# Kernel tuning notes

Hardware: AMD Instinct MI355X
Metric: run time of the kernel (lower is better)

## Reference

```python
import jax, jax.numpy as jnp
import numpy as np

B, N, DIM, H, DH = 4, 2048, 768, 12, 64

def layer_norm_no_affine(x, eps=1e-5):
    mu = jnp.mean(x, axis=-1, keepdims=True)
    var = jnp.var(x, axis=-1, keepdims=True)
    return (x - mu) / jnp.sqrt(var + eps)

def setup_inputs() -> dict:
    key = jax.random.key(0)
    ks = jax.random.split(key, 6)
    s = 1.0 / np.sqrt(DIM)
    return {
        "x": jax.random.normal(ks[0], (B, N, DIM), dtype=jnp.float32),
        "gamma": jnp.zeros((DIM,), dtype=jnp.float32),
        "Wq": jax.random.normal(ks[1], (DIM, DIM), dtype=jnp.float32) * s,
        "Wk": jax.random.normal(ks[2], (DIM, DIM), dtype=jnp.float32) * s,
        "Wv": jax.random.normal(ks[3], (DIM, DIM), dtype=jnp.float32) * s,
        "Wo": jax.random.normal(ks[4], (DIM, DIM), dtype=jnp.float32) * s,
    }

def reference(x, gamma, Wq, Wk, Wv, Wo):
    scale = DH ** -0.5
    xn = layer_norm_no_affine(x) * (gamma + 1.0)  # [b,n,dim]
    # projections (torch Linear: y = x @ W.T), split heads b n (h d) -> b h n d
    def proj(t, W):
        return (t @ W.T).reshape(B, N, H, DH).transpose(0, 2, 1, 3)
    q = proj(xn, Wq) * scale
    k = proj(xn, Wk)
    v = proj(xn, Wv)
    qk_sim = jnp.einsum('bhid,bhjd->bhij', q, k)  # full N x N scores (unfused)
    attn = jax.nn.softmax(qk_sim, axis=-1)
    out = jnp.einsum('bhij,bhjd->bhid', attn, v)
    out = out.transpose(0, 2, 1, 3).reshape(B, N, H * DH)
    return out @ Wo.T
```

## Files before the change

### kernel.cpp

```cpp
#include <hip/hip_runtime.h>
#include <stdint.h>

#define NSEQ 2048
#define NB 4
#define NH 12
#define MTOT 8192
#define DMODEL 768

typedef __attribute__((ext_vector_type(8))) short bfx8;
typedef __attribute__((ext_vector_type(4))) float fx4;

static __device__ __forceinline__ unsigned short f2bf(float f) {
  union { float f; unsigned u; } v; v.f = f;
  unsigned r = v.u + 0x7FFFu + ((v.u >> 16) & 1u);
  return (unsigned short)(r >> 16);
}

static __device__ __forceinline__ unsigned cvt_pk_bf16(float lo, float hi) {
  unsigned r;
  asm("v_cvt_pk_bf16_f32 %0, %1, %2" : "=v"(r) : "v"(lo), "v"(hi));
  return r;
}

static __device__ __forceinline__ void gload_lds16(const void* g, void* l) {
  __builtin_amdgcn_global_load_lds(
      (const __attribute__((address_space(1))) unsigned int*)g,
      (__attribute__((address_space(3))) unsigned int*)l, 16, 0, 0);
}

__global__ __launch_bounds__(256) void k_ln(const float* __restrict__ x,
                                            const float* __restrict__ gamma,
                                            unsigned short* __restrict__ xn) {
  int row = blockIdx.x * 4 + (threadIdx.x >> 6);
  int lane = threadIdx.x & 63;
  const float* xr = x + (size_t)row * DMODEL;
  float4 a = *(const float4*)(xr + lane * 4);
  float4 b = *(const float4*)(xr + 256 + lane * 4);
  float4 c = *(const float4*)(xr + 512 + lane * 4);
  float s  = a.x + a.y + a.z + a.w + b.x + b.y + b.z + b.w + c.x + c.y + c.z + c.w;
  float ss = a.x*a.x + a.y*a.y + a.z*a.z + a.w*a.w
           + b.x*b.x + b.y*b.y + b.z*b.z + b.w*b.w
           + c.x*c.x + c.y*c.y + c.z*c.z + c.w*c.w;
  #pragma unroll
  for (int off = 1; off < 64; off <<= 1) {
    s  += __shfl_xor(s, off);
    ss += __shfl_xor(ss, off);
  }
  float mu = s * (1.0f / 768.0f);
  float var = ss * (1.0f / 768.0f) - mu * mu;
  float rs = rsqrtf(var + 1e-5f);
  float4 ga = *(const float4*)(gamma + lane * 4);
  float4 gb = *(const float4*)(gamma + 256 + lane * 4);
  float4 gc = *(const float4*)(gamma + 512 + lane * 4);
  unsigned short* orow = xn + (size_t)row * DMODEL;
  ushort4 o;
  o.x = f2bf((a.x - mu) * rs * (ga.x + 1.0f));
  o.y = f2bf((a.y - mu) * rs * (ga.y + 1.0f));
  o.z = f2bf((a.z - mu) * rs * (ga.z + 1.0f));
  o.w = f2bf((a.w - mu) * rs * (ga.w + 1.0f));
  *(ushort4*)(orow + lane * 4) = o;
  o.x = f2bf((b.x - mu) * rs * (gb.x + 1.0f));
  o.y = f2bf((b.y - mu) * rs * (gb.y + 1.0f));
  o.z = f2bf((b.z - mu) * rs * (gb.z + 1.0f));
  o.w = f2bf((b.w - mu) * rs * (gb.w + 1.0f));
  *(ushort4*)(orow + 256 + lane * 4) = o;
  o.x = f2bf((c.x - mu) * rs * (gc.x + 1.0f));
  o.y = f2bf((c.y - mu) * rs * (gc.y + 1.0f));
  o.z = f2bf((c.z - mu) * rs * (gc.z + 1.0f));
  o.w = f2bf((c.w - mu) * rs * (gc.w + 1.0f));
  *(ushort4*)(orow + 512 + lane * 4) = o;
}

__global__ __launch_bounds__(256) void k_wconv(const float* __restrict__ w0,
                                               const float* __restrict__ w1,
                                               const float* __restrict__ w2,
                                               const float* __restrict__ w3,
                                               unsigned short* __restrict__ dst) {
  int which = blockIdx.y;
  const float* src = (which == 0) ? w0 : (which == 1) ? w1 : (which == 2) ? w2 : w3;
  size_t idx = ((size_t)blockIdx.x * 256 + threadIdx.x) * 4;
  float4 v = *(const float4*)(src + idx);
  ushort4 o;
  o.x = f2bf(v.x); o.y = f2bf(v.y); o.z = f2bf(v.z); o.w = f2bf(v.w);
  *(ushort4*)(dst + (size_t)which * (DMODEL * DMODEL) + idx) = o;
}

template<int MODE>
__global__ __launch_bounds__(256) void k_gemm(const unsigned short* __restrict__ A,
                                              const unsigned short* __restrict__ Bbase,
                                              unsigned short* __restrict__ q_o,
                                              unsigned short* __restrict__ k_o,
                                              unsigned short* __restrict__ v_o,
                                              float* __restrict__ f_o) {
  __shared__ unsigned short At[128 * 32];
  __shared__ unsigned short Bt[128 * 32];
  int t = threadIdx.x;
  int w = t >> 6, lane = t & 63;
  int wr = w >> 1, wc = w & 1;
  int g = lane >> 4, cc = lane & 15;
  int mbase = blockIdx.x * 128;
  int by = blockIdx.y;
  const unsigned short* Bp;
  int ncolbase;
  if (MODE == 0) {
    int which = by / 6;
    Bp = Bbase + (size_t)which * (DMODEL * DMODEL);
    ncolbase = (by % 6) * 128;
  } else {
    Bp = Bbase;
    ncolbase = by * 128;
  }
  int srow = lane >> 2;
  int schunk = (lane & 3) * 8;
  const unsigned short* Asrc = A  + (size_t)(mbase   + w * 32 + srow) * DMODEL + schunk;
  const unsigned short* Bsrc = Bp + (size_t)(ncolbase + w * 32 + srow) * DMODEL + schunk;
  unsigned short* Adst0 = At + (w * 32) * 32;
  unsigned short* Bdst0 = Bt + (w * 32) * 32;

  fx4 acc[4][4];
  #pragma unroll
  for (int i = 0; i < 4; ++i)
    #pragma unroll
    for (int j = 0; j < 4; ++j)
      acc[i][j] = (fx4){0.f, 0.f, 0.f, 0.f};

  for (int ks = 0; ks < DMODEL; ks += 32) {
    __syncthreads();
    gload_lds16(Asrc + ks,                    Adst0);
    gload_lds16(Asrc + ks + 16 * DMODEL,      Adst0 + 16 * 32);
    gload_lds16(Bsrc + ks,                    Bdst0);
    gload_lds16(Bsrc + ks + 16 * DMODEL,      Bdst0 + 16 * 32);
    __syncthreads();
    bfx8 af[4], bfr[4];
    #pragma unroll
    for (int mi = 0; mi < 4; ++mi)
      af[mi] = *(const bfx8*)(At + (wr * 64 + mi * 16 + cc) * 32 + g * 8);
    #pragma unroll
    for (int ni = 0; ni < 4; ++ni)
      bfr[ni] = *(const bfx8*)(Bt + (wc * 64 + ni * 16 + cc) * 32 + g * 8);
    #pragma unroll
    for (int mi = 0; mi < 4; ++mi)
      #pragma unroll
      for (int ni = 0; ni < 4; ++ni)
        acc[mi][ni] = __builtin_amdgcn_mfma_f32_16x16x32_bf16(af[mi], bfr[ni], acc[mi][ni], 0, 0, 0);
  }

  if (MODE == 0) {
    int which = by / 6;
    if (which < 2) {
      unsigned short* dst = (which == 0) ? q_o : k_o;
      float fs = (which == 0) ? 0.18033688f : 1.0f;
      #pragma unroll
      for (int mi = 0; mi < 4; ++mi) {
        #pragma unroll
        for (int ni = 0; ni < 4; ++ni) {
          int n = (by % 6) * 128 + wc * 64 + ni * 16 + cc;
          int h = n >> 6, dd = n & 63;
          #pragma unroll
          for (int r = 0; r < 4; ++r) {
            int m = mbase + wr * 64 + mi * 16 + g * 4 + r;
            int bb = m >> 11, nq = m & 2047;
            dst[((size_t)(bb * NH + h) * NSEQ + nq) * 64 + dd] = f2bf(acc[mi][ni][r] * fs);
          }
        }
      }
    } else {
      #pragma unroll
      for (int mi = 0; mi < 4; ++mi) {
        #pragma unroll
        for (int ni = 0; ni < 4; ++ni) {
          int n = (by % 6) * 128 + wc * 64 + ni * 16 + cc;
          int h = n >> 6, dd = n & 63;
          int m0 = mbase + wr * 64 + mi * 16 + g * 4;
          int bb = m0 >> 11, nq = m0 & 2047;
          ushort4 pk;
          pk.x = f2bf(acc[mi][ni][0]);
          pk.y = f2bf(acc[mi][ni][1]);
          pk.z = f2bf(acc[mi][ni][2]);
          pk.w = f2bf(acc[mi][ni][3]);
          *(ushort4*)(v_o + ((size_t)(bb * NH + h) * 64 + dd) * NSEQ + nq) = pk;
        }
      }
    }
  } else {
    #pragma unroll
    for (int mi = 0; mi < 4; ++mi)
      #pragma unroll
      for (int ni = 0; ni < 4; ++ni) {
        int n = by * 128 + wc * 64 + ni * 16 + cc;
        #pragma unroll
        for (int r = 0; r < 4; ++r) {
          int m = mbase + wr * 64 + mi * 16 + g * 4 + r;
          f_o[(size_t)m * DMODEL + n] = acc[mi][ni][r];
        }
      }
  }
}

__global__ __launch_bounds__(256, 3) void k_attn(const unsigned short* __restrict__ qw,
                                                 const unsigned short* __restrict__ kw,
                                                 const unsigned short* __restrict__ vtw,
                                                 unsigned short* __restrict__ ao) {
  __shared__ unsigned short Kb[2][64 * 64];
  __shared__ unsigned short Vb[2][64 * 64];
  __shared__ unsigned short Pb[4][32 * 72];
  int bid = blockIdx.x;
  int xcd = bid & 7, jj = bid >> 3;
  int bh = xcd * 6 + (jj >> 4);
  int qt = jj & 15;
  int t = threadIdx.x;
  int w = t >> 6, lane = t & 63;
  int g = lane >> 4, cc = lane & 15;
  int q0 = qt * 128 + w * 32;
  const unsigned short* qp = qw + (size_t)bh * NSEQ * 64;
  const unsigned char* kby = (const unsigned char*)(kw  + (size_t)bh * NSEQ * 64);
  const unsigned char* vby = (const unsigned char*)(vtw + (size_t)bh * 64 * NSEQ);
  unsigned short* Pw = &Pb[w][0];

  int srow = lane >> 3;
  int scol = (((lane & 7) ^ srow) << 4);
  int c0 = 2 * w, c1 = 2 * w + 1;

  auto stage = [&](int tt, int buf) {
    gload_lds16(kby + (size_t)(tt * 64 + c0 * 8 + srow) * 128 + scol, &Kb[buf][c0 * 512]);
    gload_lds16(kby + (size_t)(tt * 64 + c1 * 8 + srow) * 128 + scol, &Kb[buf][c1 * 512]);
    gload_lds16(vby + (size_t)(c0 * 8 + srow) * 4096 + tt * 128 + scol, &Vb[buf][c0 * 512]);
    gload_lds16(vby + (size_t)(c1 * 8 + srow) * 4096 + tt * 128 + scol, &Vb[buf][c1 * 512]);
  };

  bfx8 qf[2][2];
  #pragma unroll
  for (int mi = 0; mi < 2; ++mi)
    #pragma unroll
    for (int kb = 0; kb < 2; ++kb)
      qf[mi][kb] = *(const bfx8*)(qp + (size_t)(q0 + mi * 16 + cc) * 64 + kb * 32 + g * 8);

  fx4 o[4][2];
  #pragma unroll
  for (int np = 0; np < 4; ++np)
    #pragma unroll
    for (int mi = 0; mi < 2; ++mi)
      o[np][mi] = (fx4){0.f, 0.f, 0.f, 0.f};
  float l_run[2] = {0.f, 0.f};

  int col0 = (g * 16) ^ ((cc & 7) << 4);

  stage(0, 0);

  for (int tt = 0; tt < 32; ++tt) {
    int buf = tt & 1;
    __syncthreads();
    if (tt + 1 < 32) stage(tt + 1, buf ^ 1);

    bfx8 kf[4][2];
    #pragma unroll
    for (int ni = 0; ni < 4; ++ni)
      #pragma unroll
      for (int kb = 0; kb < 2; ++kb)
        kf[ni][kb] = *(const bfx8*)((const unsigned char*)&Kb[buf][0]
                                    + (ni * 16 + cc) * 128 + (col0 ^ (kb * 64)));
    fx4 st[4][2];
    #pragma unroll
    for (int ni = 0; ni < 4; ++ni)
      #pragma unroll
      for (int mi = 0; mi < 2; ++mi)
        st[ni][mi] = (fx4){0.f, 0.f, 0.f, 0.f};
    __builtin_amdgcn_s_setprio(1);
    #pragma unroll
    for (int ni = 0; ni < 4; ++ni)
      #pragma unroll
      for (int mi = 0; mi < 2; ++mi)
        #pragma unroll
        for (int kb = 0; kb < 2; ++kb)
          st[ni][mi] = __builtin_amdgcn_mfma_f32_16x16x32_bf16(kf[ni][kb], qf[mi][kb], st[ni][mi], 0, 0, 0);
    __builtin_amdgcn_s_setprio(0);

    #pragma unroll
    for (int mi = 0; mi < 2; ++mi) {
      float psum = 0.f;
      #pragma unroll
      for (int ni = 0; ni < 4; ++ni) {
        float p0 = __builtin_amdgcn_exp2f(st[ni][mi][0]);
        float p1 = __builtin_amdgcn_exp2f(st[ni][mi][1]);
        float p2 = __builtin_amdgcn_exp2f(st[ni][mi][2]);
        float p3 = __builtin_amdgcn_exp2f(st[ni][mi][3]);
        psum += (p0 + p1) + (p2 + p3);
        unsigned lo = cvt_pk_bf16(p0, p1);
        unsigned hi = cvt_pk_bf16(p2, p3);
        *(uint2*)(Pw + (mi * 16 + cc) * 72 + ni * 16 + g * 4) = make_uint2(lo, hi);
      }
      psum += __shfl_xor(psum, 16);
      psum += __shfl_xor(psum, 32);
      l_run[mi] += psum;
    }

    bfx8 vf[4][2];
    #pragma unroll
    for (int np = 0; np < 4; ++np)
      #pragma unroll
      for (int kb = 0; kb < 2; ++kb)
        vf[np][kb] = *(const bfx8*)((const unsigned char*)&Vb[buf][0]
                                    + (np * 16 + cc) * 128 + (col0 ^ (kb * 64)));

    bfx8 pf[2][2];
    #pragma unroll
    for (int mi = 0; mi < 2; ++mi)
      #pragma unroll
      for (int kb = 0; kb < 2; ++kb)
        pf[mi][kb] = *(const bfx8*)(Pw + (mi * 16 + cc) * 72 + kb * 32 + g * 8);

    __builtin_amdgcn_s_setprio(1);
    #pragma unroll
    for (int np = 0; np < 4; ++np)
      #pragma unroll
      for (int kb = 0; kb < 2; ++kb)
        #pragma unroll
        for (int mi = 0; mi < 2; ++mi)
          o[np][mi] = __builtin_amdgcn_mfma_f32_16x16x32_bf16(vf[np][kb], pf[mi][kb], o[np][mi], 0, 0, 0);
    __builtin_amdgcn_s_setprio(0);
  }

  int b = bh / NH, h = bh % NH;
  #pragma unroll
  for (int mi = 0; mi < 2; ++mi) {
    float inv = 1.0f / l_run[mi];
    int nq = q0 + mi * 16 + cc;
    unsigned short* orow = ao + (size_t)(b * NSEQ + nq) * DMODEL + h * 64;
    #pragma unroll
    for (int np = 0; np < 4; ++np) {
      ushort4 pk;
      pk.x = f2bf(o[np][mi][0] * inv);
      pk.y = f2bf(o[np][mi][1] * inv);
      pk.z = f2bf(o[np][mi][2] * inv);
      pk.w = f2bf(o[np][mi][3] * inv);
      *(ushort4*)(orow + np * 16 + g * 4) = pk;
    }
  }
}

extern "C" void kernel_launch(void* const* d_in, const int* in_sizes, int n_in,
                              void* d_out, int out_size, void* d_ws, size_t ws_size,
                              hipStream_t stream) {
  const float* x     = (const float*)d_in[0];
  const float* gamma = (const float*)d_in[1];
  const float* Wq    = (const float*)d_in[2];
  const float* Wk    = (const float*)d_in[3];
  const float* Wv    = (const float*)d_in[4];
  const float* Wo    = (const float*)d_in[5];
  float* out = (float*)d_out;

  unsigned short* xn  = (unsigned short*)d_ws;
  unsigned short* wbf = xn  + (size_t)MTOT * DMODEL;
  unsigned short* qws = wbf + (size_t)4 * DMODEL * DMODEL;
  unsigned short* kws = qws + (size_t)MTOT * DMODEL;
  unsigned short* vtws = kws + (size_t)MTOT * DMODEL;
  unsigned short* aow = vtws + (size_t)MTOT * DMODEL;

  k_ln<<<MTOT / 4, 256, 0, stream>>>(x, gamma, xn);
  k_wconv<<<dim3(576, 4), 256, 0, stream>>>(Wq, Wk, Wv, Wo, wbf);
  k_gemm<0><<<dim3(64, 18), 256, 0, stream>>>(xn, wbf, qws, kws, vtws, nullptr);
  k_attn<<<768, 256, 0, stream>>>(qws, kws, vtws, aow);
  k_gemm<1><<<dim3(64, 6), 256, 0, stream>>>(aow, wbf + (size_t)3 * DMODEL * DMODEL,
                                             nullptr, nullptr, nullptr, out);
}
```

Baseline: 158.2 us.

## Switch attention to 32x32x16 MFMA and keep P in registers via permlane32 swap

Rewrites the attention inner loop to use 32x32x16 bf16 MFMA tiles instead of 16x16x32. The transposed S^T output layout lets the probabilities be packed to bf16 and rearranged with v_permlane32_swap, so they feed the PV MFMA directly rather than going through an LDS round trip. This removes the per-wave P buffer, its LDS writes and reads, and halves the MFMA instruction count. In exchange the lane-to-element mapping becomes more intricate and a layout mistake would corrupt results.

```diff
diff --git a/kernel.cpp b/kernel.cpp
--- a/kernel.cpp
+++ b/kernel.cpp
@@ -9,6 +9,7 @@
 
 typedef __attribute__((ext_vector_type(8))) short bfx8;
 typedef __attribute__((ext_vector_type(4))) float fx4;
+typedef __attribute__((ext_vector_type(16))) float fx16;
 
 static __device__ __forceinline__ unsigned short f2bf(float f) {
   union { float f; unsigned u; } v; v.f = f;
@@ -203,47 +204,40 @@
                                                  unsigned short* __restrict__ ao) {
   __shared__ unsigned short Kb[2][64 * 64];
   __shared__ unsigned short Vb[2][64 * 64];
-  __shared__ unsigned short Pb[4][32 * 72];
   int bid = blockIdx.x;
   int xcd = bid & 7, jj = bid >> 3;
   int bh = xcd * 6 + (jj >> 4);
   int qt = jj & 15;
   int t = threadIdx.x;
   int w = t >> 6, lane = t & 63;
-  int g = lane >> 4, cc = lane & 15;
+  int c = lane & 31, b5 = lane >> 5;
   int q0 = qt * 128 + w * 32;
   const unsigned short* qp = qw + (size_t)bh * NSEQ * 64;
   const unsigned char* kby = (const unsigned char*)(kw  + (size_t)bh * NSEQ * 64);
   const unsigned char* vby = (const unsigned char*)(vtw + (size_t)bh * 64 * NSEQ);
-  unsigned short* Pw = &Pb[w][0];
 
   int srow = lane >> 3;
   int scol = (((lane & 7) ^ srow) << 4);
-  int c0 = 2 * w, c1 = 2 * w + 1;
+  int ch0 = 2 * w, ch1 = 2 * w + 1;
 
   auto stage = [&](int tt, int buf) {
-    gload_lds16(kby + (size_t)(tt * 64 + c0 * 8 + srow) * 128 + scol, &Kb[buf][c0 * 512]);
-    gload_lds16(kby + (size_t)(tt * 64 + c1 * 8 + srow) * 128 + scol, &Kb[buf][c1 * 512]);
-    gload_lds16(vby + (size_t)(c0 * 8 + srow) * 4096 + tt * 128 + scol, &Vb[buf][c0 * 512]);
-    gload_lds16(vby + (size_t)(c1 * 8 + srow) * 4096 + tt * 128 + scol, &Vb[buf][c1 * 512]);
+    gload_lds16(kby + (size_t)(tt * 64 + ch0 * 8 + srow) * 128 + scol, &Kb[buf][ch0 * 512]);
+    gload_lds16(kby + (size_t)(tt * 64 + ch1 * 8 + srow) * 128 + scol, &Kb[buf][ch1 * 512]);
+    gload_lds16(vby + (size_t)(ch0 * 8 + srow) * 4096 + tt * 128 + scol, &Vb[buf][ch0 * 512]);
+    gload_lds16(vby + (size_t)(ch1 * 8 + srow) * 4096 + tt * 128 + scol, &Vb[buf][ch1 * 512]);
   };
 
-  bfx8 qf[2][2];
-  #pragma unroll
-  for (int mi = 0; mi < 2; ++mi)
-    #pragma unroll
-    for (int kb = 0; kb < 2; ++kb)
-      qf[mi][kb] = *(const bfx8*)(qp + (size_t)(q0 + mi * 16 + cc) * 64 + kb * 32 + g * 8);
-
-  fx4 o[4][2];
-  #pragma unroll
-  for (int np = 0; np < 4; ++np)
-    #pragma unroll
-    for (int mi = 0; mi < 2; ++mi)
-      o[np][mi] = (fx4){0.f, 0.f, 0.f, 0.f};
-  float l_run[2] = {0.f, 0.f};
-
-  int col0 = (g * 16) ^ ((cc & 7) << 4);
+  bfx8 qf[4];
+  #pragma unroll
+  for (int dc = 0; dc < 4; ++dc)
+    qf[dc] = *(const bfx8*)(qp + (size_t)(q0 + c) * 64 + dc * 16 + b5 * 8);
+
+  fx16 o0, o1;
+  #pragma unroll
+  for (int i = 0; i < 16; ++i) { o0[i] = 0.f; o1[i] = 0.f; }
+  float l_run = 0.f;
+
+  int rsw = (c & 7) << 4;
 
   stage(0, 0);
 
@@ -252,89 +246,85 @@
     __syncthreads();
     if (tt + 1 < 32) stage(tt + 1, buf ^ 1);
 
-    bfx8 kf[4][2];
-    #pragma unroll
-    for (int ni = 0; ni < 4; ++ni)
-      #pragma unroll
-      for (int kb = 0; kb < 2; ++kb)
-        kf[ni][kb] = *(const bfx8*)((const unsigned char*)&Kb[buf][0]
-                                    + (ni * 16 + cc) * 128 + (col0 ^ (kb * 64)));
-    fx4 st[4][2];
-    #pragma unroll
-    for (int ni = 0; ni < 4; ++ni)
-      #pragma unroll
-      for (int mi = 0; mi < 2; ++mi)
-        st[ni][mi] = (fx4){0.f, 0.f, 0.f, 0.f};
+    const unsigned char* Kbb = (const unsigned char*)&Kb[buf][0];
+    const unsigned char* Vbb = (const unsigned char*)&Vb[buf][0];
+
+    fx16 s0, s1;
+    #pragma unroll
+    for (int i = 0; i < 16; ++i) { s0[i] = 0.f; s1[i] = 0.f; }
     __builtin_amdgcn_s_setprio(1);
     #pragma unroll
-    for (int ni = 0; ni < 4; ++ni)
-      #pragma unroll
-      for (int mi = 0; mi < 2; ++mi)
-        #pragma unroll
-        for (int kb = 0; kb < 2; ++kb)
-          st[ni][mi] = __builtin_amdgcn_mfma_f32_16x16x32_bf16(kf[ni][kb], qf[mi][kb], st[ni][mi], 0, 0, 0);
+    for (int dc = 0; dc < 4; ++dc) {
+      bfx8 kf0 = *(const bfx8*)(Kbb + (c) * 128       + ((dc * 32 + b5 * 16) ^ rsw));
+      bfx8 kf1 = *(const bfx8*)(Kbb + (32 + c) * 128  + ((dc * 32 + b5 * 16) ^ rsw));
+      s0 = __builtin_amdgcn_mfma_f32_32x32x16_bf16(kf0, qf[dc], s0, 0, 0, 0);
+      s1 = __builtin_amdgcn_mfma_f32_32x32x16_bf16(kf1, qf[dc], s1, 0, 0, 0);
+    }
     __builtin_amdgcn_s_setprio(0);
 
     #pragma unroll
-    for (int mi = 0; mi < 2; ++mi) {
-      float psum = 0.f;
-      #pragma unroll
-      for (int ni = 0; ni < 4; ++ni) {
-        float p0 = __builtin_amdgcn_exp2f(st[ni][mi][0]);
-        float p1 = __builtin_amdgcn_exp2f(st[ni][mi][1]);
-        float p2 = __builtin_amdgcn_exp2f(st[ni][mi][2]);
-        float p3 = __builtin_amdgcn_exp2f(st[ni][mi][3]);
-        psum += (p0 + p1) + (p2 + p3);
-        unsigned lo = cvt_pk_bf16(p0, p1);
-        unsigned hi = cvt_pk_bf16(p2, p3);
-        *(uint2*)(Pw + (mi * 16 + cc) * 72 + ni * 16 + g * 4) = make_uint2(lo, hi);
-      }
-      psum += __shfl_xor(psum, 16);
-      psum += __shfl_xor(psum, 32);
-      l_run[mi] += psum;
-    }
-
-    bfx8 vf[4][2];
-    #pragma unroll
-    for (int np = 0; np < 4; ++np)
-      #pragma unroll
-      for (int kb = 0; kb < 2; ++kb)
-        vf[np][kb] = *(const bfx8*)((const unsigned char*)&Vb[buf][0]
-                                    + (np * 16 + cc) * 128 + (col0 ^ (kb * 64)));
-
-    bfx8 pf[2][2];
-    #pragma unroll
-    for (int mi = 0; mi < 2; ++mi)
-      #pragma unroll
-      for (int kb = 0; kb < 2; ++kb)
-        pf[mi][kb] = *(const bfx8*)(Pw + (mi * 16 + cc) * 72 + kb * 32 + g * 8);
+    for (int i = 0; i < 16; ++i) {
+      s0[i] = __builtin_amdgcn_exp2f(s0[i]);
+      s1[i] = __builtin_amdgcn_exp2f(s1[i]);
+    }
+    float ps = 0.f;
+    #pragma unroll
+    for (int i = 0; i < 16; ++i) ps += s0[i] + s1[i];
+    ps += __shfl_xor(ps, 32);
+    l_run += ps;
+
+    bfx8 pf[4];
+    #pragma unroll
+    for (int half = 0; half < 2; ++half) {
+      {
+        unsigned w0 = cvt_pk_bf16(s0[8 * half + 0], s0[8 * half + 1]);
+        unsigned w1 = cvt_pk_bf16(s0[8 * half + 2], s0[8 * half + 3]);
+        unsigned w2 = cvt_pk_bf16(s0[8 * half + 4], s0[8 * half + 5]);
+        unsigned w3 = cvt_pk_bf16(s0[8 * half + 6], s0[8 * half + 7]);
+        asm("v_permlane32_swap_b32 %0, %1" : "+v"(w0), "+v"(w2));
+        asm("v_permlane32_swap_b32 %0, %1" : "+v"(w1), "+v"(w3));
+        uint4 u = make_uint4(w0, w1, w2, w3);
+        pf[half] = *(bfx8*)&u;
+      }
+      {
+        unsigned w0 = cvt_pk_bf16(s1[8 * half + 0], s1[8 * half + 1]);
+        unsigned w1 = cvt_pk_bf16(s1[8 * half + 2], s1[8 * half + 3]);
+        unsigned w2 = cvt_pk_bf16(s1[8 * half + 4], s1[8 * half + 5]);
+        unsigned w3 = cvt_pk_bf16(s1[8 * half + 6], s1[8 * half + 7]);
+        asm("v_permlane32_swap_b32 %0, %1" : "+v"(w0), "+v"(w2));
+        asm("v_permlane32_swap_b32 %0, %1" : "+v"(w1), "+v"(w3));
+        uint4 u = make_uint4(w0, w1, w2, w3);
+        pf[2 + half] = *(bfx8*)&u;
+      }
+    }
 
     __builtin_amdgcn_s_setprio(1);
     #pragma unroll
-    for (int np = 0; np < 4; ++np)
-      #pragma unroll
-      for (int kb = 0; kb < 2; ++kb)
-        #pragma unroll
-        for (int mi = 0; mi < 2; ++mi)
-          o[np][mi] = __builtin_amdgcn_mfma_f32_16x16x32_bf16(vf[np][kb], pf[mi][kb], o[np][mi], 0, 0, 0);
+    for (int kc = 0; kc < 4; ++kc) {
+      bfx8 vf0 = *(const bfx8*)(Vbb + (c) * 128      + ((kc * 32 + b5 * 16) ^ rsw));
+      bfx8 vf1 = *(const bfx8*)(Vbb + (32 + c) * 128 + ((kc * 32 + b5 * 16) ^ rsw));
+      o0 = __builtin_amdgcn_mfma_f32_32x32x16_bf16(vf0, pf[kc], o0, 0, 0, 0);
+      o1 = __builtin_amdgcn_mfma_f32_32x32x16_bf16(vf1, pf[kc], o1, 0, 0, 0);
+    }
     __builtin_amdgcn_s_setprio(0);
   }
 
+  float inv = 1.0f / l_run;
   int b = bh / NH, h = bh % NH;
-  #pragma unroll
-  for (int mi = 0; mi < 2; ++mi) {
-    float inv = 1.0f / l_run[mi];
-    int nq = q0 + mi * 16 + cc;
-    unsigned short* orow = ao + (size_t)(b * NSEQ + nq) * DMODEL + h * 64;
-    #pragma unroll
-    for (int np = 0; np < 4; ++np) {
-      ushort4 pk;
-      pk.x = f2bf(o[np][mi][0] * inv);
-      pk.y = f2bf(o[np][mi][1] * inv);
-      pk.z = f2bf(o[np][mi][2] * inv);
-      pk.w = f2bf(o[np][mi][3] * inv);
-      *(ushort4*)(orow + np * 16 + g * 4) = pk;
-    }
+  unsigned short* orow = ao + (size_t)(b * NSEQ + q0 + c) * DMODEL + h * 64;
+  #pragma unroll
+  for (int k = 0; k < 4; ++k) {
+    ushort4 pk;
+    pk.x = f2bf(o0[4 * k + 0] * inv);
+    pk.y = f2bf(o0[4 * k + 1] * inv);
+    pk.z = f2bf(o0[4 * k + 2] * inv);
+    pk.w = f2bf(o0[4 * k + 3] * inv);
+    *(ushort4*)(orow + 8 * k + 4 * b5) = pk;
+    pk.x = f2bf(o1[4 * k + 0] * inv);
+    pk.y = f2bf(o1[4 * k + 1] * inv);
+    pk.z = f2bf(o1[4 * k + 2] * inv);
+    pk.w = f2bf(o1[4 * k + 3] * inv);
+    *(ushort4*)(orow + 32 + 8 * k + 4 * b5) = pk;
   }
 }
 
```

After: 154.7 us. -2.2%, faster.
